# Kernel tuning notes

Hardware: AMD Instinct MI355X
Metric: run time of the kernel (lower is better)

The kernel has to match this reference:

```python
import jax, jax.numpy as jnp
import numpy as np

B, S, D = 32, 2048, 1024
H = 8
D_ATTN = 256
D_HEAD = D_ATTN // H          # 32
D_HEAD_OUT = D // H           # 128
SOFTMAX_TEMP = 1.0


def setup_inputs() -> dict:
    key = jax.random.key(0)
    k0, k1, k2, k3, k4 = jax.random.split(key, 5)
    features = jax.random.normal(k0, (B, S, D), dtype=jnp.float32)
    # truncated-normal(std=0.01) init approximated with scaled normal
    w1 = jax.random.normal(k1, (H, D, D_HEAD), dtype=jnp.float32) * 0.01
    b1 = jax.random.normal(k2, (H, D_HEAD), dtype=jnp.float32) * 0.01
    w2 = jax.random.normal(k3, (H, D_HEAD, D_HEAD_OUT), dtype=jnp.float32) * 0.01
    b2 = jax.random.normal(k4, (H, D_HEAD_OUT), dtype=jnp.float32) * 0.01
    return {"features": features, "w1": w1, "b1": b1, "w2": w2, "b2": b2}


def reference(features, w1, b1, w2, b2):
    Bc, Sc, Dc = features.shape
    # per-head first projection: [B,H,S,d_head]
    h = jnp.einsum('bsd,hde->bhse', features, w1) + b1[None, :, None, :]
    h = jax.nn.gelu(h, approximate=False)  # torch nn.GELU default is exact erf
    # second projection: [B,H,S,d_head_out]
    logits = jnp.einsum('bhse,heo->bhso', h, w2) + b2[None, :, None, :]
    # softmax over seq dim (axis=2)
    smw = jax.nn.softmax(logits / SOFTMAX_TEMP, axis=2)
    # [B,H,S,D/H] -> [B,S,H,D/H] -> [B,S,D]
    smw = smw.transpose(0, 2, 1, 3).reshape(Bc, Sc, Dc)
    return (features * smw).sum(axis=1)  # [B,D]
```

## Files before the change

### kernel.cpp

```cpp
#include <hip/hip_runtime.h>
#include <math.h>

#define S_  2048
#define D_  1024

typedef __attribute__((ext_vector_type(8))) short short8;
typedef __attribute__((ext_vector_type(4))) float f32x4;

static __device__ __forceinline__ unsigned short f2bf(float x) {
    unsigned int u = __builtin_bit_cast(unsigned int, x);
    u += 0x7fffu + ((u >> 16) & 1u);
    return (unsigned short)(u >> 16);
}

__device__ __forceinline__ void gl_lds16(const void* g, void* l) {
    __builtin_amdgcn_global_load_lds(
        (const __attribute__((address_space(1))) unsigned int*)g,
        (__attribute__((address_space(3))) unsigned int*)l, 16, 0, 0);
}

__global__ void prep_w1(const float* __restrict__ w1, short* __restrict__ w1p) {
    int tid = blockIdx.x * 256 + threadIdx.x;
    int lane = tid & 63;
    int fragid = tid >> 6;
    int cf = fragid & 15, ks = fragid >> 4;
    int col = cf * 16 + (lane & 15);
    int h = col >> 5, e = col & 31;
    int d0 = ks * 32 + (lane >> 4) * 8;
    short8 v;
#pragma unroll
    for (int r = 0; r < 8; ++r)
        v[r] = (short)f2bf(w1[((size_t)h * D_ + (d0 + r)) * 32 + e]);
    *(short8*)(w1p + (size_t)tid * 8) = v;
}

__global__ void prep_w2(const float* __restrict__ w2, short* __restrict__ w2p) {
    int tid = blockIdx.x * 256 + threadIdx.x;
    int lane = tid & 63;
    int fragid = tid >> 6;
    int cf2 = fragid & 7, h = fragid >> 3;
    int o = cf2 * 16 + (lane & 15);
    int e0 = (lane >> 4) * 8;
    short8 v;
#pragma unroll
    for (int r = 0; r < 8; ++r)
        v[r] = (short)f2bf(w2[((size_t)h * 32 + (e0 + r)) * 128 + o]);
    *(short8*)(w2p + (size_t)tid * 8) = v;
}

__global__ __launch_bounds__(256, 4) void fused1(
        const float* __restrict__ feat,
        const short* __restrict__ w1p,
        const short* __restrict__ w2p,
        const float* __restrict__ b1,
        const float* __restrict__ b2,
        float* __restrict__ pnum,
        float* __restrict__ pden)
{
    __shared__ __align__(16) char lds[34816];
    short* Bbuf = (short*)lds;
    short* hact = (short*)lds;

    const int tid = threadIdx.x;
    const int wv = tid >> 6;
    const int lane = tid & 63;
    const int lr = lane & 15;
    const int lg = lane >> 4;
    const int wr = wv >> 1, wc = wv & 1;
    const size_t m0 = (size_t)blockIdx.x * 64;

    const f32x4* Arow0 = (const f32x4*)(feat + (m0 + (size_t)(wr * 32 + lr)) * D_);
    const f32x4* Arow1 = (const f32x4*)(feat + (m0 + (size_t)(wr * 32 + 16 + lr)) * D_);

    const f32x4 vzero = {0.f, 0.f, 0.f, 0.f};
    f32x4 acc[2][8];
#pragma unroll
    for (int i = 0; i < 2; ++i)
#pragma unroll
        for (int j = 0; j < 8; ++j) acc[i][j] = vzero;

    auto stageB = [&](int buf_, int ks_) {
#pragma unroll
        for (int j = 0; j < 4; ++j)
            gl_lds16(w1p + (size_t)ks_ * 8192 + (size_t)(j * 256 + tid) * 8,
                     Bbuf + buf_ * 8192 + (j * 256 + wv * 64) * 8);
    };

    stageB(0, 0);
    f32x4 p00 = Arow0[lg * 2], p01 = Arow0[lg * 2 + 1];
    f32x4 p10 = Arow1[lg * 2], p11 = Arow1[lg * 2 + 1];
    int buf = 0;
    for (int ks = 0; ks < 32; ++ks) {
        __syncthreads();
        if (ks + 1 < 32) stageB(buf ^ 1, ks + 1);
        f32x4 a00 = p00, a01 = p01, a10 = p10, a11 = p11;
        if (ks + 1 < 32) {
            const int o = (ks + 1) * 8 + lg * 2;
            p00 = Arow0[o]; p01 = Arow0[o + 1];
            p10 = Arow1[o]; p11 = Arow1[o + 1];
        }
        short8 af0, af1;
        af0[0] = (short)f2bf(a00.x); af0[1] = (short)f2bf(a00.y);
        af0[2] = (short)f2bf(a00.z); af0[3] = (short)f2bf(a00.w);
        af0[4] = (short)f2bf(a01.x); af0[5] = (short)f2bf(a01.y);
        af0[6] = (short)f2bf(a01.z); af0[7] = (short)f2bf(a01.w);
        af1[0] = (short)f2bf(a10.x); af1[1] = (short)f2bf(a10.y);
        af1[2] = (short)f2bf(a10.z); af1[3] = (short)f2bf(a10.w);
        af1[4] = (short)f2bf(a11.x); af1[5] = (short)f2bf(a11.y);
        af1[6] = (short)f2bf(a11.z); af1[7] = (short)f2bf(a11.w);

        const short8* Bf = (const short8*)(Bbuf + buf * 8192);
#pragma unroll
        for (int cf = 0; cf < 8; ++cf) {
            short8 bfr = Bf[(wc * 8 + cf) * 64 + lane];
            acc[0][cf] = __builtin_amdgcn_mfma_f32_16x16x32_bf16(af0, bfr, acc[0][cf], 0, 0, 0);
            acc[1][cf] = __builtin_amdgcn_mfma_f32_16x16x32_bf16(af1, bfr, acc[1][cf], 0, 0, 0);
        }
        buf ^= 1;
    }

    __syncthreads();

#pragma unroll
    for (int rf1 = 0; rf1 < 2; ++rf1)
#pragma unroll
    for (int cf = 0; cf < 8; ++cf) {
        const int col = wc * 128 + cf * 16 + lr;
        const float bias = b1[col];
#pragma unroll
        for (int r = 0; r < 4; ++r) {
            const int row = wr * 32 + rf1 * 16 + lg * 4 + r;
            float x = acc[rf1][cf][r] + bias;
            float g = 0.5f * x * (1.0f + erff(x * 0.70710678118654752f));
            hact[row * 264 + col] = (short)f2bf(g);
        }
    }
    __syncthreads();

    float bias2[16];
#pragma unroll
    for (int cf = 0; cf < 16; ++cf) {
        const int h = 2 * wv + (cf >> 3);
        bias2[cf] = b2[h * 128 + (cf & 7) * 16 + lr];
    }
    float num_acc[16], den_acc[16];
#pragma unroll
    for (int cf = 0; cf < 16; ++cf) { num_acc[cf] = 0.f; den_acc[cf] = 0.f; }

    for (int rf = 0; rf < 4; ++rf) {
        short8 ah0 = *(const short8*)(hact + (rf * 16 + lr) * 264 + (2 * wv + 0) * 32 + lg * 8);
        short8 ah1 = *(const short8*)(hact + (rf * 16 + lr) * 264 + (2 * wv + 1) * 32 + lg * 8);
#pragma unroll
        for (int cf = 0; cf < 16; ++cf) {
            const int h = 2 * wv + (cf >> 3);
            short8 bw = *(const short8*)(w2p + ((size_t)(h * 8 + (cf & 7)) * 64 + lane) * 8);
            f32x4 c = vzero;
            c = __builtin_amdgcn_mfma_f32_16x16x32_bf16((cf < 8) ? ah0 : ah1, bw, c, 0, 0, 0);
            const int col = wv * 256 + (cf >> 3) * 128 + (cf & 7) * 16 + lr;
#pragma unroll
            for (int r = 0; r < 4; ++r) {
                const float e = __expf(c[r] + bias2[cf]);
                const int row = rf * 16 + lg * 4 + r;
                const float f = feat[(m0 + row) * D_ + col];
                den_acc[cf] += e;
                num_acc[cf] = fmaf(f, e, num_acc[cf]);
            }
        }
    }

    const size_t pb = (size_t)blockIdx.x * 1024;
#pragma unroll
    for (int cf = 0; cf < 16; ++cf) {
        float dn = den_acc[cf];
        dn += __shfl_xor(dn, 16); dn += __shfl_xor(dn, 32);
        float nm = num_acc[cf];
        nm += __shfl_xor(nm, 16); nm += __shfl_xor(nm, 32);
        if (lg == 0) {
            const int col = wv * 256 + (cf >> 3) * 128 + (cf & 7) * 16 + lr;
            pden[pb + col] = dn;
            pnum[pb + col] = nm;
        }
    }
}

__global__ __launch_bounds__(256) void finalize2(
        const float* __restrict__ pnum,
        const float* __restrict__ pden,
        float* __restrict__ out)
{
    const int idx = blockIdx.x * 256 + threadIdx.x;
    const int b = idx >> 10;
    const int d = idx & 1023;
    const size_t base = (size_t)b * 32 * 1024 + d;
    float n = 0.f, dn = 0.f;
#pragma unroll 8
    for (int j = 0; j < 32; ++j) {
        n  += pnum[base + (size_t)j * 1024];
        dn += pden[base + (size_t)j * 1024];
    }
    out[idx] = n / dn;
}

extern "C" void kernel_launch(void* const* d_in, const int* in_sizes, int n_in,
                              void* d_out, int out_size, void* d_ws, size_t ws_size,
                              hipStream_t stream) {
    (void)in_sizes; (void)n_in; (void)out_size; (void)ws_size;
    const float* feat = (const float*)d_in[0];
    const float* w1   = (const float*)d_in[1];
    const float* b1   = (const float*)d_in[2];
    const float* w2   = (const float*)d_in[3];
    const float* b2   = (const float*)d_in[4];
    float* out = (float*)d_out;

    char* ws = (char*)d_ws;
    float* pnum = (float*)ws;
    float* pden = (float*)(ws + (4ull << 20));
    short* w1p  = (short*)(ws + (8ull << 20));
    short* w2p  = (short*)(ws + (8ull << 20) + (512ull << 10));

    prep_w1<<<128, 256, 0, stream>>>(w1, w1p);
    prep_w2<<<16, 256, 0, stream>>>(w2, w2p);
    fused1<<<1024, 256, 0, stream>>>(feat, w1p, w2p, b1, b2, pnum, pden);
    finalize2<<<128, 256, 0, stream>>>(pnum, pden, out);
}
```

Before: 174.2 us.

## Triple-buffer W1 staging and stage exp weights in LDS for coalesced reduction

Replaces the double-buffered K loop with a three-stage ring of LDS buffers and two register A prefetch sets, synchronised by explicit vmcnt waits and barriers, so global loads run further ahead of the MFMAs. The epilogue now handles 16-row chunks one at a time. Each chunk's GELU activations and bf16-rounded exp values go through LDS, so the feature-weighted reduction uses coalesced float4 loads per thread instead of strided scalar reads. This costs more LDS (48KB, occupancy hint lowered to 3 blocks), extra barriers, and bf16 rounding of the softmax numerator and denominator weights.

New measurement: 199.2 us. 1.14x slower.

```diff
diff --git a/kernel.cpp b/kernel.cpp
--- a/kernel.cpp
+++ b/kernel.cpp
@@ -11,6 +11,10 @@
     unsigned int u = __builtin_bit_cast(unsigned int, x);
     u += 0x7fffu + ((u >> 16) & 1u);
     return (unsigned short)(u >> 16);
+}
+static __device__ __forceinline__ float bf2f(unsigned short s) {
+    unsigned int u = ((unsigned int)s) << 16;
+    return __builtin_bit_cast(float, u);
 }
 
 __device__ __forceinline__ void gl_lds16(const void* g, void* l) {
@@ -48,7 +52,7 @@
     *(short8*)(w2p + (size_t)tid * 8) = v;
 }
 
-__global__ __launch_bounds__(256, 4) void fused1(
+__global__ __launch_bounds__(256, 3) void fused1(
         const float* __restrict__ feat,
         const short* __restrict__ w1p,
         const short* __restrict__ w2p,
@@ -57,9 +61,10 @@
         float* __restrict__ pnum,
         float* __restrict__ pden)
 {
-    __shared__ __align__(16) char lds[34816];
+    __shared__ __align__(16) char lds[49152];
     short* Bbuf = (short*)lds;
-    short* hact = (short*)lds;
+    short* hact16 = (short*)lds;
+    unsigned short* Est = (unsigned short*)(lds + 8448);
 
     const int tid = threadIdx.x;
     const int wv = tid >> 6;
@@ -85,102 +90,135 @@
             gl_lds16(w1p + (size_t)ks_ * 8192 + (size_t)(j * 256 + tid) * 8,
                      Bbuf + buf_ * 8192 + (j * 256 + wv * 64) * 8);
     };
-
-    stageB(0, 0);
-    f32x4 p00 = Arow0[lg * 2], p01 = Arow0[lg * 2 + 1];
-    f32x4 p10 = Arow1[lg * 2], p11 = Arow1[lg * 2 + 1];
-    int buf = 0;
-    for (int ks = 0; ks < 32; ++ks) {
-        __syncthreads();
-        if (ks + 1 < 32) stageB(buf ^ 1, ks + 1);
-        f32x4 a00 = p00, a01 = p01, a10 = p10, a11 = p11;
-        if (ks + 1 < 32) {
-            const int o = (ks + 1) * 8 + lg * 2;
-            p00 = Arow0[o]; p01 = Arow0[o + 1];
-            p10 = Arow1[o]; p11 = Arow1[o + 1];
-        }
-        short8 af0, af1;
-        af0[0] = (short)f2bf(a00.x); af0[1] = (short)f2bf(a00.y);
-        af0[2] = (short)f2bf(a00.z); af0[3] = (short)f2bf(a00.w);
-        af0[4] = (short)f2bf(a01.x); af0[5] = (short)f2bf(a01.y);
-        af0[6] = (short)f2bf(a01.z); af0[7] = (short)f2bf(a01.w);
-        af1[0] = (short)f2bf(a10.x); af1[1] = (short)f2bf(a10.y);
-        af1[2] = (short)f2bf(a10.z); af1[3] = (short)f2bf(a10.w);
-        af1[4] = (short)f2bf(a11.x); af1[5] = (short)f2bf(a11.y);
-        af1[6] = (short)f2bf(a11.z); af1[7] = (short)f2bf(a11.w);
-
-        const short8* Bf = (const short8*)(Bbuf + buf * 8192);
+    f32x4 pfA[4], pfB[4];
+    auto loadA = [&](f32x4* pf, int ks_) {
+        const int o = ks_ * 8 + lg * 2;
+        pf[0] = Arow0[o]; pf[1] = Arow0[o + 1];
+        pf[2] = Arow1[o]; pf[3] = Arow1[o + 1];
+    };
+    auto mkfrag = [&](const f32x4* pf, short8& af0, short8& af1) {
+        af0[0] = (short)f2bf(pf[0].x); af0[1] = (short)f2bf(pf[0].y);
+        af0[2] = (short)f2bf(pf[0].z); af0[3] = (short)f2bf(pf[0].w);
+        af0[4] = (short)f2bf(pf[1].x); af0[5] = (short)f2bf(pf[1].y);
+        af0[6] = (short)f2bf(pf[1].z); af0[7] = (short)f2bf(pf[1].w);
+        af1[0] = (short)f2bf(pf[2].x); af1[1] = (short)f2bf(pf[2].y);
+        af1[2] = (short)f2bf(pf[2].z); af1[3] = (short)f2bf(pf[2].w);
+        af1[4] = (short)f2bf(pf[3].x); af1[5] = (short)f2bf(pf[3].y);
+        af1[6] = (short)f2bf(pf[3].z); af1[7] = (short)f2bf(pf[3].w);
+    };
+    auto kcompute = [&](int bufI, const short8& af0, const short8& af1) {
+        const short8* Bf = (const short8*)(Bbuf + bufI * 8192);
 #pragma unroll
         for (int cf = 0; cf < 8; ++cf) {
             short8 bfr = Bf[(wc * 8 + cf) * 64 + lane];
             acc[0][cf] = __builtin_amdgcn_mfma_f32_16x16x32_bf16(af0, bfr, acc[0][cf], 0, 0, 0);
             acc[1][cf] = __builtin_amdgcn_mfma_f32_16x16x32_bf16(af1, bfr, acc[1][cf], 0, 0, 0);
         }
-        buf ^= 1;
-    }
-
+    };
+
+    stageB(0, 0); loadA(pfA, 0);
+    stageB(1, 1); loadA(pfB, 1);
+
+    int cur = 0;
+    for (int kk = 0; kk < 15; ++kk) {
+        const int ks = kk * 2;
+        asm volatile("s_waitcnt vmcnt(8)" ::: "memory");
+        __builtin_amdgcn_s_barrier();
+        {
+            int nb = cur + 2; if (nb >= 3) nb -= 3;
+            stageB(nb, ks + 2);
+            short8 af0, af1; mkfrag(pfA, af0, af1);
+            loadA(pfA, ks + 2);
+            kcompute(cur, af0, af1);
+            cur = (cur == 2) ? 0 : cur + 1;
+        }
+        asm volatile("s_waitcnt vmcnt(8)" ::: "memory");
+        __builtin_amdgcn_s_barrier();
+        {
+            int nb = cur + 2; if (nb >= 3) nb -= 3;
+            stageB(nb, ks + 3);
+            short8 af0, af1; mkfrag(pfB, af0, af1);
+            loadA(pfB, ks + 3);
+            kcompute(cur, af0, af1);
+            cur = (cur == 2) ? 0 : cur + 1;
+        }
+    }
+    asm volatile("s_waitcnt vmcnt(8)" ::: "memory");
+    __builtin_amdgcn_s_barrier();
+    {
+        short8 af0, af1; mkfrag(pfA, af0, af1);
+        kcompute(cur, af0, af1);
+        cur = (cur == 2) ? 0 : cur + 1;
+    }
+    asm volatile("s_waitcnt vmcnt(0)" ::: "memory");
+    __builtin_amdgcn_s_barrier();
+    {
+        short8 af0, af1; mkfrag(pfB, af0, af1);
+        kcompute(cur, af0, af1);
+    }
     __syncthreads();
 
-#pragma unroll
-    for (int rf1 = 0; rf1 < 2; ++rf1)
-#pragma unroll
-    for (int cf = 0; cf < 8; ++cf) {
-        const int col = wc * 128 + cf * 16 + lr;
-        const float bias = b1[col];
-#pragma unroll
-        for (int r = 0; r < 4; ++r) {
-            const int row = wr * 32 + rf1 * 16 + lg * 4 + r;
-            float x = acc[rf1][cf][r] + bias;
-            float g = 0.5f * x * (1.0f + erff(x * 0.70710678118654752f));
-            hact[row * 264 + col] = (short)f2bf(g);
-        }
-    }
-    __syncthreads();
-
     float bias2[16];
 #pragma unroll
-    for (int cf = 0; cf < 16; ++cf) {
-        const int h = 2 * wv + (cf >> 3);
-        bias2[cf] = b2[h * 128 + (cf & 7) * 16 + lr];
-    }
-    float num_acc[16], den_acc[16];
-#pragma unroll
-    for (int cf = 0; cf < 16; ++cf) { num_acc[cf] = 0.f; den_acc[cf] = 0.f; }
+    for (int cf = 0; cf < 16; ++cf)
+        bias2[cf] = b2[(2 * wv + (cf >> 3)) * 128 + (cf & 7) * 16 + lr];
+
+    const int c0 = tid * 4;
+    f32x4 nacc = vzero, dacc = vzero;
 
     for (int rf = 0; rf < 4; ++rf) {
-        short8 ah0 = *(const short8*)(hact + (rf * 16 + lr) * 264 + (2 * wv + 0) * 32 + lg * 8);
-        short8 ah1 = *(const short8*)(hact + (rf * 16 + lr) * 264 + (2 * wv + 1) * 32 + lg * 8);
+        if (wr == (rf >> 1)) {
+            const int a = rf & 1;
+#pragma unroll
+            for (int cf = 0; cf < 8; ++cf) {
+                const int col = wc * 128 + cf * 16 + lr;
+                const float bias = b1[col];
+#pragma unroll
+                for (int r = 0; r < 4; ++r) {
+                    float x = acc[a][cf][r] + bias;
+                    float g = 0.5f * x * (1.0f + erff(x * 0.70710678118654752f));
+                    hact16[(lg * 4 + r) * 264 + col] = (short)f2bf(g);
+                }
+            }
+        }
+        __syncthreads();
+
+        short8 ah0 = *(const short8*)(hact16 + lr * 264 + (2 * wv + 0) * 32 + lg * 8);
+        short8 ah1 = *(const short8*)(hact16 + lr * 264 + (2 * wv + 1) * 32 + lg * 8);
 #pragma unroll
         for (int cf = 0; cf < 16; ++cf) {
             const int h = 2 * wv + (cf >> 3);
             short8 bw = *(const short8*)(w2p + ((size_t)(h * 8 + (cf & 7)) * 64 + lane) * 8);
             f32x4 c = vzero;
             c = __builtin_amdgcn_mfma_f32_16x16x32_bf16((cf < 8) ? ah0 : ah1, bw, c, 0, 0, 0);
-            const int col = wv * 256 + (cf >> 3) * 128 + (cf & 7) * 16 + lr;
+            const int colL = wv * 256 + (cf >> 3) * 128 + (cf & 7) * 16 + lr;
 #pragma unroll
             for (int r = 0; r < 4; ++r) {
-                const float e = __expf(c[r] + bias2[cf]);
-                const int row = rf * 16 + lg * 4 + r;
-                const float f = feat[(m0 + row) * D_ + col];
-                den_acc[cf] += e;
-                num_acc[cf] = fmaf(f, e, num_acc[cf]);
+                float e = __expf(c[r] + bias2[cf]);
+                Est[(lg * 4 + r) * 1032 + colL] = f2bf(e);
             }
         }
-    }
-
-    const size_t pb = (size_t)blockIdx.x * 1024;
-#pragma unroll
-    for (int cf = 0; cf < 16; ++cf) {
-        float dn = den_acc[cf];
-        dn += __shfl_xor(dn, 16); dn += __shfl_xor(dn, 32);
-        float nm = num_acc[cf];
-        nm += __shfl_xor(nm, 16); nm += __shfl_xor(nm, 32);
-        if (lg == 0) {
-            const int col = wv * 256 + (cf >> 3) * 128 + (cf & 7) * 16 + lr;
-            pden[pb + col] = dn;
-            pnum[pb + col] = nm;
-        }
-    }
+        __syncthreads();
+
+        const float* fb = feat + (m0 + (size_t)rf * 16) * D_ + c0;
+#pragma unroll
+        for (int row = 0; row < 16; ++row) {
+            f32x4 fv = *(const f32x4*)(fb + (size_t)row * D_);
+            unsigned long long ev = *(const unsigned long long*)(Est + row * 1032 + c0);
+            f32x4 e;
+            e.x = bf2f((unsigned short)(ev));
+            e.y = bf2f((unsigned short)(ev >> 16));
+            e.z = bf2f((unsigned short)(ev >> 32));
+            e.w = bf2f((unsigned short)(ev >> 48));
+            dacc += e;
+            nacc += fv * e;
+        }
+        __syncthreads();
+    }
+
+    const size_t pb = (size_t)blockIdx.x * 1024 + c0;
+    *(f32x4*)(pnum + pb) = nacc;
+    *(f32x4*)(pden + pb) = dacc;
 }
 
 __global__ __launch_bounds__(256) void finalize2(
```

## Split fused kernel into GEMM1 and GEMM2+weighted-sum kernels via global bf16 activations

Applied to the files above, without the earlier changes.

The single fused kernel is split in two. The first writes the bf16 GELU activations to a global workspace. The second, with 16-row blocks and 4096 of them, computes the second projection and exp, stages the exp values in LDS as bf16, and does coalesced float4 feature reads for the weighted sums. Finalize now reduces 128 partials instead of 32. The aim is to remove the strided, uncoalesced feature loads and the low parallelism of the fused epilogue, at the cost of an extra global round-trip for the activations, bf16 rounding of the exp weights, and a third launch.

Result: slower. 213.2 us (+22.4%).

```diff
diff --git a/kernel.cpp b/kernel.cpp
--- a/kernel.cpp
+++ b/kernel.cpp
@@ -1,4 +1,5 @@
 #include <hip/hip_runtime.h>
+#include <hip/hip_bf16.h>
 #include <math.h>
 
 #define S_  2048
@@ -7,10 +8,12 @@
 typedef __attribute__((ext_vector_type(8))) short short8;
 typedef __attribute__((ext_vector_type(4))) float f32x4;
 
-static __device__ __forceinline__ unsigned short f2bf(float x) {
-    unsigned int u = __builtin_bit_cast(unsigned int, x);
-    u += 0x7fffu + ((u >> 16) & 1u);
-    return (unsigned short)(u >> 16);
+static __device__ __forceinline__ short f2bf(float x) {
+    return __builtin_bit_cast(short, __float2bfloat16(x));
+}
+static __device__ __forceinline__ float bf2f(unsigned short s) {
+    unsigned int u = ((unsigned int)s) << 16;
+    return __builtin_bit_cast(float, u);
 }
 
 __device__ __forceinline__ void gl_lds16(const void* g, void* l) {
@@ -30,7 +33,7 @@
     short8 v;
 #pragma unroll
     for (int r = 0; r < 8; ++r)
-        v[r] = (short)f2bf(w1[((size_t)h * D_ + (d0 + r)) * 32 + e]);
+        v[r] = f2bf(w1[((size_t)h * D_ + (d0 + r)) * 32 + e]);
     *(short8*)(w1p + (size_t)tid * 8) = v;
 }
 
@@ -44,22 +47,19 @@
     short8 v;
 #pragma unroll
     for (int r = 0; r < 8; ++r)
-        v[r] = (short)f2bf(w2[((size_t)h * 32 + (e0 + r)) * 128 + o]);
+        v[r] = f2bf(w2[((size_t)h * 32 + (e0 + r)) * 128 + o]);
     *(short8*)(w2p + (size_t)tid * 8) = v;
 }
 
-__global__ __launch_bounds__(256, 4) void fused1(
+__global__ __launch_bounds__(256) void gemm1(
         const float* __restrict__ feat,
         const short* __restrict__ w1p,
-        const short* __restrict__ w2p,
         const float* __restrict__ b1,
-        const float* __restrict__ b2,
-        float* __restrict__ pnum,
-        float* __restrict__ pden)
+        short* __restrict__ hact)
 {
     __shared__ __align__(16) char lds[34816];
     short* Bbuf = (short*)lds;
-    short* hact = (short*)lds;
+    short* hstage = (short*)lds;
 
     const int tid = threadIdx.x;
     const int wv = tid >> 6;
@@ -86,40 +86,35 @@
                      Bbuf + buf_ * 8192 + (j * 256 + wv * 64) * 8);
     };
 
+    f32x4 p0, p1, p2, p3;
+    auto loadA = [&](int ks_) {
+        const int o = ks_ * 8 + lg * 2;
+        p0 = Arow0[o]; p1 = Arow0[o + 1];
+        p2 = Arow1[o]; p3 = Arow1[o + 1];
+    };
+
     stageB(0, 0);
-    f32x4 p00 = Arow0[lg * 2], p01 = Arow0[lg * 2 + 1];
-    f32x4 p10 = Arow1[lg * 2], p11 = Arow1[lg * 2 + 1];
-    int buf = 0;
+    loadA(0);
+    __syncthreads();
+
     for (int ks = 0; ks < 32; ++ks) {
-        __syncthreads();
-        if (ks + 1 < 32) stageB(buf ^ 1, ks + 1);
-        f32x4 a00 = p00, a01 = p01, a10 = p10, a11 = p11;
-        if (ks + 1 < 32) {
-            const int o = (ks + 1) * 8 + lg * 2;
-            p00 = Arow0[o]; p01 = Arow0[o + 1];
-            p10 = Arow1[o]; p11 = Arow1[o + 1];
-        }
+        if (ks < 31) stageB((ks & 1) ^ 1, ks + 1);
         short8 af0, af1;
-        af0[0] = (short)f2bf(a00.x); af0[1] = (short)f2bf(a00.y);
-        af0[2] = (short)f2bf(a00.z); af0[3] = (short)f2bf(a00.w);
-        af0[4] = (short)f2bf(a01.x); af0[5] = (short)f2bf(a01.y);
-        af0[6] = (short)f2bf(a01.z); af0[7] = (short)f2bf(a01.w);
-        af1[0] = (short)f2bf(a10.x); af1[1] = (short)f2bf(a10.y);
-        af1[2] = (short)f2bf(a10.z); af1[3] = (short)f2bf(a10.w);
-        af1[4] = (short)f2bf(a11.x); af1[5] = (short)f2bf(a11.y);
-        af1[6] = (short)f2bf(a11.z); af1[7] = (short)f2bf(a11.w);
-
-        const short8* Bf = (const short8*)(Bbuf + buf * 8192);
+        af0[0] = f2bf(p0.x); af0[1] = f2bf(p0.y); af0[2] = f2bf(p0.z); af0[3] = f2bf(p0.w);
+        af0[4] = f2bf(p1.x); af0[5] = f2bf(p1.y); af0[6] = f2bf(p1.z); af0[7] = f2bf(p1.w);
+        af1[0] = f2bf(p2.x); af1[1] = f2bf(p2.y); af1[2] = f2bf(p2.z); af1[3] = f2bf(p2.w);
+        af1[4] = f2bf(p3.x); af1[5] = f2bf(p3.y); af1[6] = f2bf(p3.z); af1[7] = f2bf(p3.w);
+        if (ks < 31) loadA(ks + 1);
+
+        const short8* Bf = (const short8*)(Bbuf + (ks & 1) * 8192);
 #pragma unroll
         for (int cf = 0; cf < 8; ++cf) {
             short8 bfr = Bf[(wc * 8 + cf) * 64 + lane];
             acc[0][cf] = __builtin_amdgcn_mfma_f32_16x16x32_bf16(af0, bfr, acc[0][cf], 0, 0, 0);
             acc[1][cf] = __builtin_amdgcn_mfma_f32_16x16x32_bf16(af1, bfr, acc[1][cf], 0, 0, 0);
         }
-        buf ^= 1;
-    }
-
-    __syncthreads();
+        __syncthreads();
+    }
 
 #pragma unroll
     for (int rf1 = 0; rf1 < 2; ++rf1)
@@ -132,58 +127,90 @@
             const int row = wr * 32 + rf1 * 16 + lg * 4 + r;
             float x = acc[rf1][cf][r] + bias;
             float g = 0.5f * x * (1.0f + erff(x * 0.70710678118654752f));
-            hact[row * 264 + col] = (short)f2bf(g);
+            hstage[row * 264 + col] = f2bf(g);
         }
     }
     __syncthreads();
+#pragma unroll
+    for (int it = 0; it < 8; ++it) {
+        const int idx = it * 256 + tid;
+        const int row = idx >> 5;
+        const int c8 = idx & 31;
+        short8 v = *(const short8*)(hstage + row * 264 + c8 * 8);
+        *(short8*)(hact + (m0 + row) * 256 + c8 * 8) = v;
+    }
+}
+
+__global__ __launch_bounds__(256) void gemm2w(
+        const short* __restrict__ hact,
+        const float* __restrict__ feat,
+        const short* __restrict__ w2p,
+        const float* __restrict__ b2,
+        float* __restrict__ pnum,
+        float* __restrict__ pden)
+{
+    __shared__ __align__(16) char lds[41216];
+    short* hstage = (short*)lds;
+    unsigned short* Est = (unsigned short*)(lds + 8192);
+
+    const int tid = threadIdx.x;
+    const int wv = tid >> 6;
+    const int lane = tid & 63;
+    const int lr = lane & 15;
+    const int lg = lane >> 4;
+    const size_t m0 = (size_t)blockIdx.x * 16;
+
+#pragma unroll
+    for (int j = 0; j < 2; ++j)
+        gl_lds16(hact + m0 * 256 + (size_t)(j * 256 + tid) * 8,
+                 hstage + (j * 256 + wv * 64) * 8);
 
     float bias2[16];
+#pragma unroll
+    for (int cf = 0; cf < 16; ++cf)
+        bias2[cf] = b2[(2 * wv + (cf >> 3)) * 128 + (cf & 7) * 16 + lr];
+
+    __syncthreads();
+
+    short8 ah0 = *(const short8*)(hstage + lr * 256 + (2 * wv + 0) * 32 + lg * 8);
+    short8 ah1 = *(const short8*)(hstage + lr * 256 + (2 * wv + 1) * 32 + lg * 8);
+    const f32x4 vzero = {0.f, 0.f, 0.f, 0.f};
 #pragma unroll
     for (int cf = 0; cf < 16; ++cf) {
         const int h = 2 * wv + (cf >> 3);
-        bias2[cf] = b2[h * 128 + (cf & 7) * 16 + lr];
-    }
-    float num_acc[16], den_acc[16];
-#pragma unroll
-    for (int cf = 0; cf < 16; ++cf) { num_acc[cf] = 0.f; den_acc[cf] = 0.f; }
-
-    for (int rf = 0; rf < 4; ++rf) {
-        short8 ah0 = *(const short8*)(hact + (rf * 16 + lr) * 264 + (2 * wv + 0) * 32 + lg * 8);
-        short8 ah1 = *(const short8*)(hact + (rf * 16 + lr) * 264 + (2 * wv + 1) * 32 + lg * 8);
-#pragma unroll
-        for (int cf = 0; cf < 16; ++cf) {
-            const int h = 2 * wv + (cf >> 3);
-            short8 bw = *(const short8*)(w2p + ((size_t)(h * 8 + (cf & 7)) * 64 + lane) * 8);
-            f32x4 c = vzero;
-            c = __builtin_amdgcn_mfma_f32_16x16x32_bf16((cf < 8) ? ah0 : ah1, bw, c, 0, 0, 0);
-            const int col = wv * 256 + (cf >> 3) * 128 + (cf & 7) * 16 + lr;
-#pragma unroll
-            for (int r = 0; r < 4; ++r) {
-                const float e = __expf(c[r] + bias2[cf]);
-                const int row = rf * 16 + lg * 4 + r;
-                const float f = feat[(m0 + row) * D_ + col];
-                den_acc[cf] += e;
-                num_acc[cf] = fmaf(f, e, num_acc[cf]);
-            }
+        short8 bw = *(const short8*)(w2p + ((size_t)(h * 8 + (cf & 7)) * 64 + lane) * 8);
+        f32x4 c = vzero;
+        c = __builtin_amdgcn_mfma_f32_16x16x32_bf16((cf < 8) ? ah0 : ah1, bw, c, 0, 0, 0);
+        const int colL = wv * 256 + (cf >> 3) * 128 + (cf & 7) * 16 + lr;
+#pragma unroll
+        for (int r = 0; r < 4; ++r) {
+            float e = __expf(c[r] + bias2[cf]);
+            Est[(lg * 4 + r) * 1032 + colL] = (unsigned short)f2bf(e);
         }
     }
-
-    const size_t pb = (size_t)blockIdx.x * 1024;
-#pragma unroll
-    for (int cf = 0; cf < 16; ++cf) {
-        float dn = den_acc[cf];
-        dn += __shfl_xor(dn, 16); dn += __shfl_xor(dn, 32);
-        float nm = num_acc[cf];
-        nm += __shfl_xor(nm, 16); nm += __shfl_xor(nm, 32);
-        if (lg == 0) {
-            const int col = wv * 256 + (cf >> 3) * 128 + (cf & 7) * 16 + lr;
-            pden[pb + col] = dn;
-            pnum[pb + col] = nm;
-        }
-    }
-}
-
-__global__ __launch_bounds__(256) void finalize2(
+    __syncthreads();
+
+    const int c0 = tid * 4;
+    f32x4 nacc = vzero, dacc = vzero;
+    const float* fb = feat + m0 * D_ + c0;
+#pragma unroll
+    for (int row = 0; row < 16; ++row) {
+        f32x4 fv = *(const f32x4*)(fb + (size_t)row * D_);
+        unsigned long long ev = *(const unsigned long long*)(Est + row * 1032 + c0);
+        f32x4 e;
+        e.x = bf2f((unsigned short)(ev));
+        e.y = bf2f((unsigned short)(ev >> 16));
+        e.z = bf2f((unsigned short)(ev >> 32));
+        e.w = bf2f((unsigned short)(ev >> 48));
+        dacc += e;
+        nacc += fv * e;
+    }
+    const size_t pb = (size_t)blockIdx.x * 1024 + c0;
+    *(f32x4*)(pnum + pb) = nacc;
+    *(f32x4*)(pden + pb) = dacc;
+}
+
+__global__ __launch_bounds__(256) void finalize3(
         const float* __restrict__ pnum,
         const float* __restrict__ pden,
         float* __restrict__ out)
@@ -191,10 +218,9 @@
     const int idx = blockIdx.x * 256 + threadIdx.x;
     const int b = idx >> 10;
     const int d = idx & 1023;
-    const size_t base = (size_t)b * 32 * 1024 + d;
+    const size_t base = (size_t)b * 128 * 1024 + d;
     float n = 0.f, dn = 0.f;
-#pragma unroll 8
-    for (int j = 0; j < 32; ++j) {
+    for (int j = 0; j < 128; ++j) {
         n  += pnum[base + (size_t)j * 1024];
         dn += pden[base + (size_t)j * 1024];
     }
@@ -213,13 +239,15 @@
     float* out = (float*)d_out;
 
     char* ws = (char*)d_ws;
-    float* pnum = (float*)ws;
-    float* pden = (float*)(ws + (4ull << 20));
-    short* w1p  = (short*)(ws + (8ull << 20));
-    short* w2p  = (short*)(ws + (8ull << 20) + (512ull << 10));
+    short* hact = (short*)ws;
+    float* pnum = (float*)(ws + (32ull << 20));
+    float* pden = (float*)(ws + (48ull << 20));
+    short* w1p  = (short*)(ws + (64ull << 20));
+    short* w2p  = (short*)(ws + (64ull << 20) + (512ull << 10));
 
     prep_w1<<<128, 256, 0, stream>>>(w1, w1p);
     prep_w2<<<16, 256, 0, stream>>>(w2, w2p);
-    fused1<<<1024, 256, 0, stream>>>(feat, w1p, w2p, b1, b2, pnum, pden);
-    finalize2<<<128, 256, 0, stream>>>(pnum, pden, out);
-}
+    gemm1<<<1024, 256, 0, stream>>>(feat, w1p, b1, hact);
+    gemm2w<<<4096, 256, 0, stream>>>(hact, feat, w2p, b2, pnum, pden);
+    finalize3<<<128, 256, 0, stream>>>(pnum, pden, out);
+}
```
